# Performance work log

Hardware: AMD Instinct MI355X
Metric: run time of the kernel (lower is better)

Reference implementation:

```python
import jax, jax.numpy as jnp
import numpy as np

B, L, D, H = 8, 1024, 512, 8  # L must equal len_ for the skew trick
DH = D // H


def setup_inputs() -> dict:
    key = jax.random.key(0)
    ks = jax.random.split(key, 6)
    s = 0.02
    return {
        "x": jax.random.normal(ks[0], (B, L, D), dtype=jnp.float32),
        "Wq": jax.random.normal(ks[1], (D, D), dtype=jnp.float32) * s,
        "Wk": jax.random.normal(ks[2], (D, D), dtype=jnp.float32) * s,
        "Wv": jax.random.normal(ks[3], (D, D), dtype=jnp.float32) * s,
        "We": jax.random.normal(ks[4], (L, DH), dtype=jnp.float32) * s,  # e_projection weight: (len_, d_head)
        "Wo": jax.random.normal(ks[5], (D, D), dtype=jnp.float32) * s,
        "bo": jnp.zeros((D,), dtype=jnp.float32),
        "unused": 0,
    }


def reference(x, Wq, Wk, Wv, We, Wo, bo, unused):
    Bx, Lx, Dx = x.shape
    q = (x @ Wq.T).reshape(Bx, Lx, H, DH)  # blhd
    k = (x @ Wk.T).reshape(Bx, Lx, H, DH)
    v = (x @ Wv.T).reshape(Bx, Lx, H, DH)

    # relative-position logits: e_projection(q) then permute -> (B, H, L, len_)
    qe = jnp.einsum('blhd,ed->bhle', q, We)

    # 'skew' trick: reflect-pad right by L-1, zero-pad (right 1, bottom L-1),
    # reshape (B,H,2L-1,2L) -> (B,H,2L,2L-1), slice [:L, L-1:] -> (B,H,L,L)
    qe = jnp.pad(qe, ((0, 0), (0, 0), (0, 0), (0, Lx - 1)), mode='reflect')
    qe = jnp.pad(qe, ((0, 0), (0, 0), (0, Lx - 1), (0, 1)))
    qe = qe.reshape(Bx, H, 2 * Lx, 2 * Lx - 1)
    s_rel = qe[:, :, :Lx, Lx - 1:]

    scale = 1.0 / jnp.sqrt(jnp.asarray(DH, dtype=x.dtype))
    scores = jnp.einsum('blhd,bshd->bhls', q, k)
    A = jax.nn.softmax(scale * (scores + s_rel), axis=-1)
    V = jnp.einsum('bhls,bshd->blhd', A, v).reshape(Bx, Lx, Dx)
    return V @ Wo.T + bo
```

## Files before the change

kernel.cpp:

```cpp
#include <hip/hip_runtime.h>

#define Lc 1024
#define Dc 512
#define Hc 8
#define DHc 64

typedef __attribute__((ext_vector_type(8))) short bf16x8;
typedef __attribute__((ext_vector_type(4))) float f32x4;
typedef __attribute__((ext_vector_type(16))) float f32x16;

typedef __attribute__((address_space(1))) const unsigned int guint;
typedef __attribute__((address_space(3))) unsigned int luint;

__device__ __forceinline__ void gload_lds16(const void* g, void* l) {
    __builtin_amdgcn_global_load_lds((guint*)g, (luint*)l, 16, 0, 0);
}

__device__ __forceinline__ unsigned short f2bf(float f) {
    unsigned u = __float_as_uint(f);
    u += 0x7fffu + ((u >> 16) & 1u);
    return (unsigned short)(u >> 16);
}
__device__ __forceinline__ unsigned pk2(float a, float b) {
    return (unsigned)f2bf(a) | ((unsigned)f2bf(b) << 16);
}
__device__ __forceinline__ unsigned pk2t(float a, float b) {
    return __builtin_amdgcn_perm(__float_as_uint(b), __float_as_uint(a), 0x07060302u);
}
__device__ __forceinline__ float bf2f(unsigned short s) { return __uint_as_float(((unsigned)s) << 16); }

__device__ __forceinline__ void pl32swap(unsigned &a, unsigned &b) {
    asm volatile("v_permlane32_swap_b32 %0, %1" : "+v"(a), "+v"(b));
}
__device__ __forceinline__ unsigned alignbit(unsigned hi, unsigned lo, unsigned sh) {
    unsigned d;
    asm("v_alignbit_b32 %0, %1, %2, %3" : "=v"(d) : "v"(hi), "v"(lo), "v"(sh));
    return d;
}

__global__ void cvt_all_kernel(
    const float* __restrict__ x,  const float* __restrict__ Wq,
    const float* __restrict__ Wk, const float* __restrict__ Wv,
    const float* __restrict__ Wo, const float* __restrict__ We,
    unsigned short* __restrict__ xb,  unsigned short* __restrict__ wqb,
    unsigned short* __restrict__ wkb, unsigned short* __restrict__ wvb,
    unsigned short* __restrict__ wob, unsigned short* __restrict__ wet)
{
    int bid = blockIdx.x;
    const float* src; unsigned short* dst; size_t base;
    if      (bid < 2048) { src = x;  dst = xb;  base = (size_t)bid * 2048; }
    else if (bid < 2176) { src = Wq; dst = wqb; base = (size_t)(bid-2048) * 2048; }
    else if (bid < 2304) { src = Wk; dst = wkb; base = (size_t)(bid-2176) * 2048; }
    else if (bid < 2432) { src = Wv; dst = wvb; base = (size_t)(bid-2304) * 2048; }
    else if (bid < 2560) { src = Wo; dst = wob; base = (size_t)(bid-2432) * 2048; }
    else                 { src = We; dst = wet; base = (size_t)(bid-2560) * 2048; }
    size_t i = base + (size_t)threadIdx.x * 8;
    float4 a = *(const float4*)&src[i];
    float4 b = *(const float4*)&src[i + 4];
    uint4 o = make_uint4(pk2(a.x, a.y), pk2(a.z, a.w), pk2(b.x, b.y), pk2(b.z, b.w));
    *(uint4*)&dst[i] = o;
}

__global__ __launch_bounds__(256, 3) void proj_mfma_kernel(
    const unsigned short* __restrict__ xb,
    const unsigned short* __restrict__ wq, const unsigned short* __restrict__ wk,
    const unsigned short* __restrict__ wv,
    unsigned short* __restrict__ qo, unsigned short* __restrict__ ko,
    unsigned short* __restrict__ vtg, float qscale)
{
    const unsigned short* W;
    if (blockIdx.z == 0)      W = wq;
    else if (blockIdx.z == 1) W = wk;
    else                      W = wv;

    __shared__ unsigned short smem[128 * 136];
    unsigned short* As = smem;
    unsigned short* Bs = smem + 8192;

    const int t = threadIdx.x;
    const int lane = t & 63, w = t >> 6;
    const int lq = lane >> 4, ln = lane & 15;
    const int m0 = blockIdx.y * 128, n0 = blockIdx.x * 128;
    const int wm = (w & 1) * 64, wn = (w >> 1) * 64;
    const int srow = t >> 3;
    const int lsg  = ((t & 7) ^ ((t >> 3) & 7)) * 8;
    const int key  = ln & 7;

    f32x4 acc[4][4];
    #pragma unroll
    for (int i = 0; i < 4; i++)
        #pragma unroll
        for (int j = 0; j < 4; j++) acc[i][j] = (f32x4){0.f,0.f,0.f,0.f};

    for (int c0 = 0; c0 < 512; c0 += 64) {
        __syncthreads();
        #pragma unroll
        for (int g = 0; g < 4; g++) {
            gload_lds16(&xb[(size_t)(m0 + 32*g + srow) * 512 + c0 + lsg], &As[(32*g + srow)*64 + (t&7)*8]);
            gload_lds16(&W [(size_t)(n0 + 32*g + srow) * 512 + c0 + lsg], &Bs[(32*g + srow)*64 + (t&7)*8]);
        }
        __syncthreads();

        #pragma unroll
        for (int kk = 0; kk < 2; kk++) {
            bf16x8 af[4], bf[4];
            #pragma unroll
            for (int i = 0; i < 4; i++)
                af[i] = *(bf16x8*)&As[(wm + 16*i + ln)*64 + ((kk*4 + lq) ^ key)*8];
            #pragma unroll
            for (int j = 0; j < 4; j++)
                bf[j] = *(bf16x8*)&Bs[(wn + 16*j + ln)*64 + ((kk*4 + lq) ^ key)*8];
            #pragma unroll
            for (int i = 0; i < 4; i++)
                #pragma unroll
                for (int j = 0; j < 4; j++)
                    acc[i][j] = __builtin_amdgcn_mfma_f32_16x16x32_bf16(af[i], bf[j], acc[i][j], 0, 0, 0);
        }
    }

    if (blockIdx.z < 2) {
        unsigned short* out = (blockIdx.z == 0) ? qo : ko;
        const float osc = (blockIdx.z == 0) ? qscale : 1.0f;
        #pragma unroll
        for (int i = 0; i < 4; i++) {
            #pragma unroll
            for (int r = 0; r < 4; r++) {
                int m = m0 + wm + 16*i + 4*lq + r;
                int b = m >> 10, l = m & 1023;
                #pragma unroll
                for (int j = 0; j < 4; j++) {
                    int n = n0 + wn + 16*j + ln;
                    int h = n >> 6, dh = n & 63;
                    out[((size_t)((b*Hc + h)*Lc + l))*DHc + dh] = f2bf(acc[i][j][r] * osc);
                }
            }
        }
    } else {
        __syncthreads();
        unsigned short* Ts = smem;
        #pragma unroll
        for (int i = 0; i < 4; i++) {
            int mlb = wm + 16*i + 4*lq;
            #pragma unroll
            for (int j = 0; j < 4; j++) {
                int nl = wn + 16*j + ln;
                *(uint2*)&Ts[nl*136 + mlb] = make_uint2(pk2(acc[i][j][0], acc[i][j][1]),
                                                        pk2(acc[i][j][2], acc[i][j][3]));
            }
        }
        __syncthreads();
        const int b = m0 >> 10, l0m = m0 & 1023;
        const int nl = t >> 1, seg = (t & 1) * 64;
        const int ng = n0 + nl, h = ng >> 6, dh = ng & 63;
        unsigned short* dst = vtg + (((size_t)(b*Hc + h))*DHc + dh)*Lc + l0m + seg;
        #pragma unroll
        for (int u = 0; u < 8; u++)
            *(uint4*)&dst[8*u] = *(uint4*)&Ts[nl*136 + seg + 8*u];
    }
}

__global__ __launch_bounds__(256, 2) void out_mfma_kernel(
    const unsigned short* __restrict__ A, const unsigned short* __restrict__ W,
    const float* __restrict__ bias, float* __restrict__ out)
{
    __shared__ unsigned short As[128 * 64];
    __shared__ unsigned short Bs[64 * 64];

    const int t = threadIdx.x;
    const int lane = t & 63, w = t >> 6;
    const int lq = lane >> 4, ln = lane & 15;
    const int m0 = blockIdx.y * 128, n0 = blockIdx.x * 64;
    const int wm = (w & 1) * 64, wn = (w >> 1) * 32;
    const int srow = t >> 3;
    const int lsg  = ((t & 7) ^ ((t >> 3) & 7)) * 8;
    const int key  = ln & 7;

    f32x4 acc[4][2];
    #pragma unroll
    for (int i = 0; i < 4; i++)
        #pragma unroll
        for (int j = 0; j < 2; j++) acc[i][j] = (f32x4){0.f,0.f,0.f,0.f};

    for (int c0 = 0; c0 < 512; c0 += 64) {
        __syncthreads();
        #pragma unroll
        for (int g = 0; g < 4; g++)
            gload_lds16(&A[(size_t)(m0 + 32*g + srow) * 512 + c0 + lsg], &As[(32*g + srow)*64 + (t&7)*8]);
        #pragma unroll
        for (int g = 0; g < 2; g++)
            gload_lds16(&W[(size_t)(n0 + 32*g + srow) * 512 + c0 + lsg], &Bs[(32*g + srow)*64 + (t&7)*8]);
        __syncthreads();

        #pragma unroll
        for (int kk = 0; kk < 2; kk++) {
            bf16x8 af[4], bf[2];
            #pragma unroll
            for (int i = 0; i < 4; i++)
                af[i] = *(bf16x8*)&As[(wm + 16*i + ln)*64 + ((kk*4 + lq) ^ key)*8];
            #pragma unroll
            for (int j = 0; j < 2; j++)
                bf[j] = *(bf16x8*)&Bs[(wn + 16*j + ln)*64 + ((kk*4 + lq) ^ key)*8];
            #pragma unroll
            for (int i = 0; i < 4; i++)
                #pragma unroll
                for (int j = 0; j < 2; j++)
                    acc[i][j] = __builtin_amdgcn_mfma_f32_16x16x32_bf16(af[i], bf[j], acc[i][j], 0, 0, 0);
        }
    }

    float bb[2];
    #pragma unroll
    for (int j = 0; j < 2; j++) bb[j] = bias[n0 + wn + 16*j + ln];

    #pragma unroll
    for (int i = 0; i < 4; i++) {
        #pragma unroll
        for (int r = 0; r < 4; r++) {
            int m = m0 + wm + 16*i + 4*lq + r;
            #pragma unroll
            for (int j = 0; j < 2; j++) {
                int n = n0 + wn + 16*j + ln;
                out[(size_t)m * Dc + n] = acc[i][j][r] + bb[j];
            }
        }
    }
}

__global__ __launch_bounds__(256, 4) void attn_v13_kernel(
    const unsigned short* __restrict__ q, const unsigned short* __restrict__ k,
    const unsigned short* __restrict__ vtg, const unsigned short* __restrict__ wet,
    unsigned short* __restrict__ attn)
{
    __shared__ unsigned short smem[20480];
    unsigned short* ksp  = smem;
    unsigned short* vtp  = smem + 4096;
    unsigned short* wesp = smem + 8192;
    unsigned short* qes  = smem + 12288;

    const int t    = threadIdx.x;
    const int lane = t & 63, w = t >> 6;
    const int ln31 = lane & 31, hi = lane >> 5;
    const int si   = w >> 1;
    const int li   = w & 1;

    const int n   = blockIdx.x;
    const int xcd = n & 7, idx = n >> 3;
    const int bh  = xcd * 8 + (idx >> 4);
    const int l0  = (idx & 15) * 64;

    const unsigned short* qb  = q   + (size_t)bh * (Lc * DHc);
    const unsigned short* kb  = k   + (size_t)bh * (Lc * DHc);
    const unsigned short* vtb = vtg + (size_t)bh * (DHc * Lc);

    const int srow2 = t >> 3;
    const int lsg2  = ((t & 7) ^ ((t >> 3) & 7)) * 8;
    const int k7    = ln31 & 7;
    const int lloc  = 32*li + ln31;
    const int wkey  = (lloc & 15) << 2;
    unsigned short* qrow = &qes[lloc * 128];

    bf16x8 qf[4];
    #pragma unroll
    for (int kk = 0; kk < 4; kk++)
        qf[kk] = *(const bf16x8*)&qb[(size_t)(l0 + lloc)*64 + kk*16 + hi*8];

    const int pb0 = 15 - (l0 >> 6);

    gload_lds16(&wet[(size_t)(64*pb0 + srow2)*64 + lsg2],        &vtp [t*8]);
    gload_lds16(&wet[(size_t)(64*pb0 + 32 + srow2)*64 + lsg2],   &vtp [2048 + t*8]);
    gload_lds16(&wet[(size_t)(64*(pb0+1) + srow2)*64 + lsg2],    &wesp[t*8]);
    gload_lds16(&wet[(size_t)(64*(pb0+1) + 32 + srow2)*64 + lsg2], &wesp[2048 + t*8]);
    gload_lds16(&kb [(size_t)srow2*64 + lsg2],                   &ksp [t*8]);
    gload_lds16(&kb [(size_t)(32 + srow2)*64 + lsg2],            &ksp [2048 + t*8]);
    __syncthreads();

    {
        f32x16 qec = (f32x16){0.f,0.f,0.f,0.f,0.f,0.f,0.f,0.f,0.f,0.f,0.f,0.f,0.f,0.f,0.f,0.f};
        #pragma unroll
        for (int kk = 0; kk < 4; kk++) {
            bf16x8 wf = *(bf16x8*)&vtp[(32*si + ln31)*64 + ((2*kk + hi) ^ k7)*8];
            qec = __builtin_amdgcn_mfma_f32_32x32x16_bf16(wf, qf[kk], qec, 0, 0, 0);
        }
        const int cb = (pb0 & 1) * 64;
        #pragma unroll
        for (int g = 0; g < 4; g++) {
            const int col = (cb + 32*si + 8*g + 4*hi) ^ wkey;
            *(uint2*)&qrow[col] = make_uint2(pk2(qec[4*g], qec[4*g+1]),
                                             pk2(qec[4*g+2], qec[4*g+3]));
        }
    }

    f32x16 Ov[2];
    #pragma unroll
    for (int dt = 0; dt < 2; dt++)
        Ov[dt] = (f32x16){0.f,0.f,0.f,0.f,0.f,0.f,0.f,0.f,0.f,0.f,0.f,0.f,0.f,0.f,0.f,0.f};
    float Lacc = 0.f;

    int pbOld = pb0 - 1;

    #pragma unroll 1
    for (int s0 = 0; s0 < Lc; s0 += 64) {
        const int c0  = l0 - s0;
        const int ac0 = c0 < 0 ? -c0 : c0;
        const int pb  = (960 - ac0) >> 6;
        const int newp = (pb > pbOld) ? pb + 1 : pb;
        pbOld = pb;
        const int cb = (newp & 1) * 64;
        const bool more = (s0 < Lc - 64);
        const int nc  = c0 - 64;
        const int nac = nc < 0 ? -nc : nc;
        const int npb = (960 - nac) >> 6;
        const int nnp = (npb > pb) ? npb + 1 : npb;

        __syncthreads();

        gload_lds16(&vtb[(size_t)srow2*1024 + s0 + lsg2],        &vtp[t*8]);
        gload_lds16(&vtb[(size_t)(32 + srow2)*1024 + s0 + lsg2], &vtp[2048 + t*8]);

        {
            f32x16 qec = (f32x16){0.f,0.f,0.f,0.f,0.f,0.f,0.f,0.f,0.f,0.f,0.f,0.f,0.f,0.f,0.f,0.f};
            #pragma unroll
            for (int kk = 0; kk < 4; kk++) {
                bf16x8 wf = *(bf16x8*)&wesp[(32*si + ln31)*64 + ((2*kk + hi) ^ k7)*8];
                qec = __builtin_amdgcn_mfma_f32_32x32x16_bf16(wf, qf[kk], qec, 0, 0, 0);
            }
            #pragma unroll
            for (int g = 0; g < 4; g++) {
                const int col = (cb + 32*si + 8*g + 4*hi) ^ wkey;
                *(uint2*)&qrow[col] = make_uint2(pk2(qec[4*g], qec[4*g+1]),
                                                 pk2(qec[4*g+2], qec[4*g+3]));
            }
        }

        __syncthreads();

        if (more) {
            gload_lds16(&wet[(size_t)(64*nnp + srow2)*64 + lsg2],      &wesp[t*8]);
            gload_lds16(&wet[(size_t)(64*nnp + 32 + srow2)*64 + lsg2], &wesp[2048 + t*8]);
        }

        f32x16 sc = (f32x16){0.f,0.f,0.f,0.f,0.f,0.f,0.f,0.f,0.f,0.f,0.f,0.f,0.f,0.f,0.f,0.f};
        #pragma unroll
        for (int kk = 0; kk < 4; kk++) {
            bf16x8 kf = *(bf16x8*)&ksp[(32*si + ln31)*64 + ((2*kk + hi) ^ k7)*8];
            sc = __builtin_amdgcn_mfma_f32_32x32x16_bf16(kf, qf[kk], sc, 0, 0, 0);
        }

        float p[16];
        if (c0 >= 128 || c0 <= -64) {
            const bool asc = (c0 >= 128);
            #pragma unroll
            for (int g = 0; g < 4; g++) {
                const int dbase0 = c0 + lloc - (32*si + 8*g + 4*hi);
                const int base = asc ? (1023 - dbase0) : (1020 + dbase0);
                const int a  = (base & ~3) & 127;
                const int a2 = (a + 4) & 127;
                const uint2 w01 = *(const uint2*)&qrow[a  ^ wkey];
                const uint2 w23 = *(const uint2*)&qrow[a2 ^ wkey];
                const int off = base & 3;
                const bool oh = (off >= 2);
                const unsigned wl = oh ? w01.y : w01.x;
                const unsigned wm = oh ? w23.x : w01.y;
                const unsigned wh = oh ? w23.y : w23.x;
                const unsigned sh = (unsigned)(off & 1) * 16u;
                const unsigned r0 = alignbit(wm, wl, sh);
                const unsigned r1 = alignbit(wh, wm, sh);
                float b0, b1, b2, b3;
                if (asc) {
                    b0 = __uint_as_float(r0 << 16);
                    b1 = __uint_as_float(r0 & 0xffff0000u);
                    b2 = __uint_as_float(r1 << 16);
                    b3 = __uint_as_float(r1 & 0xffff0000u);
                } else {
                    b0 = __uint_as_float(r1 & 0xffff0000u);
                    b1 = __uint_as_float(r1 << 16);
                    b2 = __uint_as_float(r0 & 0xffff0000u);
                    b3 = __uint_as_float(r0 << 16);
                }
                p[4*g+0] = __builtin_amdgcn_exp2f(sc[4*g+0] + b0);
                p[4*g+1] = __builtin_amdgcn_exp2f(sc[4*g+1] + b1);
                p[4*g+2] = __builtin_amdgcn_exp2f(sc[4*g+2] + b2);
                p[4*g+3] = __builtin_amdgcn_exp2f(sc[4*g+3] + b3);
            }
        } else {
            #pragma unroll
            for (int g = 0; g < 4; g++) {
                const int sb = 32*si + 8*g + 4*hi;
                #pragma unroll
                for (int r = 0; r < 4; r++) {
                    int d  = c0 + lloc - sb - r;
                    int ad = d < 0 ? -d : d;
                    int m  = 1023 - ad;
                    float bias = bf2f(qrow[(m & 127) ^ wkey]);
                    p[4*g + r] = __builtin_amdgcn_exp2f(sc[4*g + r] + bias);
                }
            }
        }

        {
            float t0 = (p[0]+p[1]) + (p[2]+p[3]);
            float t1 = (p[4]+p[5]) + (p[6]+p[7]);
            float t2 = (p[8]+p[9]) + (p[10]+p[11]);
            float t3 = (p[12]+p[13]) + (p[14]+p[15]);
            Lacc += (t0 + t1) + (t2 + t3);
        }
        unsigned d0[4], d1[4];
        #pragma unroll
        for (int g = 0; g < 4; g++) {
            d0[g] = pk2t(p[4*g],     p[4*g + 1]);
            d1[g] = pk2t(p[4*g + 2], p[4*g + 3]);
        }
        bf16x8 pfr[2];
        #pragma unroll
        for (int kk = 0; kk < 2; kk++) {
            pl32swap(d0[2*kk], d0[2*kk + 1]);
            pl32swap(d1[2*kk], d1[2*kk + 1]);
            uint4 fu = make_uint4(d0[2*kk], d1[2*kk], d0[2*kk + 1], d1[2*kk + 1]);
            pfr[kk] = *(bf16x8*)&fu;
        }

        __syncthreads();

        if (more) {
            gload_lds16(&kb[(size_t)(s0 + 64 + srow2)*64 + lsg2],      &ksp[t*8]);
            gload_lds16(&kb[(size_t)(s0 + 64 + 32 + srow2)*64 + lsg2], &ksp[2048 + t*8]);
        }

        #pragma unroll
        for (int kk = 0; kk < 2; kk++)
            #pragma unroll
            for (int dt = 0; dt < 2; dt++) {
                bf16x8 vf = *(bf16x8*)&vtp[(32*dt + ln31)*64 + (((4*si + 2*kk + hi) ^ k7))*8];
                Ov[dt] = __builtin_amdgcn_mfma_f32_32x32x16_bf16(vf, pfr[kk], Ov[dt], 0, 0, 0);
            }
    }

    unsigned la = __float_as_uint(Lacc), lb = la;
    pl32swap(la, lb);
    float Lh = Lacc + __uint_as_float(hi ? la : lb);

    __syncthreads();
    float* scr = (float*)smem;
    if (si == 1) {
        #pragma unroll
        for (int dt = 0; dt < 2; dt++)
            #pragma unroll
            for (int rg = 0; rg < 16; rg++)
                scr[(dt*16 + rg)*128 + li*64 + lane] = Ov[dt][rg];
        scr[32*128 + li*64 + lane] = Lh;
    }
    __syncthreads();
    if (si == 0) {
        const float Lt = Lh + scr[32*128 + li*64 + lane];
        const float inv = 1.f / Lt;
        const int b = bh >> 3, h = bh & 7;
        const int lg = l0 + lloc;
        unsigned short* dst = attn + ((size_t)(b*Lc + lg))*Dc + h*DHc;
        #pragma unroll
        for (int dt = 0; dt < 2; dt++)
            #pragma unroll
            for (int g = 0; g < 4; g++) {
                float v0 = (Ov[dt][4*g]   + scr[(dt*16 + 4*g)*128 + li*64 + lane]) * inv;
                float v1 = (Ov[dt][4*g+1] + scr[(dt*16 + 4*g+1)*128 + li*64 + lane]) * inv;
                float v2 = (Ov[dt][4*g+2] + scr[(dt*16 + 4*g+2)*128 + li*64 + lane]) * inv;
                float v3 = (Ov[dt][4*g+3] + scr[(dt*16 + 4*g+3)*128 + li*64 + lane]) * inv;
                *(uint2*)&dst[32*dt + 8*g + 4*hi] = make_uint2(pk2(v0, v1), pk2(v2, v3));
            }
    }
}

extern "C" void kernel_launch(void* const* d_in, const int* in_sizes, int n_in,
                              void* d_out, int out_size, void* d_ws, size_t ws_size,
                              hipStream_t stream)
{
    (void)in_sizes; (void)n_in; (void)out_size; (void)ws_size;
    const float* x  = (const float*)d_in[0];
    const float* Wq = (const float*)d_in[1];
    const float* Wk = (const float*)d_in[2];
    const float* Wv = (const float*)d_in[3];
    const float* We = (const float*)d_in[4];
    const float* Wo = (const float*)d_in[5];
    const float* bo = (const float*)d_in[6];

    const size_t NT = (size_t)8 * Hc * Lc * DHc;
    unsigned short* qw  = (unsigned short*)d_ws;
    unsigned short* kw  = qw  + NT;
    unsigned short* vtg = kw  + NT;
    unsigned short* xbf = vtg + NT;
    unsigned short* awb = xbf + NT;
    unsigned short* wqb = awb + NT;
    unsigned short* wkb = wqb + 262144;
    unsigned short* wvb = wkb + 262144;
    unsigned short* wob = wvb + 262144;
    unsigned short* wet = wob + 262144;

    cvt_all_kernel<<<2592, 256, 0, stream>>>(x, Wq, Wk, Wv, Wo, We,
                                             xbf, wqb, wkb, wvb, wob, wet);
    proj_mfma_kernel<<<dim3(4, 64, 3), 256, 0, stream>>>(xbf, wqb, wkb, wvb,
                                                         qw, kw, vtg,
                                                         0.125f * 1.44269504089f);
    attn_v13_kernel<<<1024, 256, 0, stream>>>(qw, kw, vtg, wet, awb);
    out_mfma_kernel<<<dim3(8, 64), 256, 0, stream>>>(awb, wob, bo, (float*)d_out);
}
```

Measured before the change: 162.6 us.

## Fuse Q/K/V projections into one kernel sharing the x tile

Merges the three separate Q, K and V projection GEMM launches (grid z=3) into a single kernel in which each block loads one 128x64 x tile and multiplies it against 64-column tiles of Wq, Wk and Wv. Each x tile is read from global memory and staged in LDS once instead of three times. In exchange the grid shrinks from 768 to 512 blocks, the N tile per weight drops from 128 to 64, occupancy falls from 3 to 2 blocks per CU, and each thread holds more accumulators.

```diff
diff --git a/kernel.cpp b/kernel.cpp
--- a/kernel.cpp
+++ b/kernel.cpp
@@ -61,66 +61,78 @@
     *(uint4*)&dst[i] = o;
 }
 
-__global__ __launch_bounds__(256, 3) void proj_mfma_kernel(
+__global__ __launch_bounds__(256, 2) void proj_fused_kernel(
     const unsigned short* __restrict__ xb,
     const unsigned short* __restrict__ wq, const unsigned short* __restrict__ wk,
     const unsigned short* __restrict__ wv,
     unsigned short* __restrict__ qo, unsigned short* __restrict__ ko,
     unsigned short* __restrict__ vtg, float qscale)
 {
-    const unsigned short* W;
-    if (blockIdx.z == 0)      W = wq;
-    else if (blockIdx.z == 1) W = wk;
-    else                      W = wv;
-
-    __shared__ unsigned short smem[128 * 136];
+    __shared__ unsigned short smem[20480];
     unsigned short* As = smem;
-    unsigned short* Bs = smem + 8192;
+    unsigned short* Bs0 = smem + 8192;
+    unsigned short* Bs1 = smem + 12288;
+    unsigned short* Bs2 = smem + 16384;
 
     const int t = threadIdx.x;
     const int lane = t & 63, w = t >> 6;
     const int lq = lane >> 4, ln = lane & 15;
-    const int m0 = blockIdx.y * 128, n0 = blockIdx.x * 128;
-    const int wm = (w & 1) * 64, wn = (w >> 1) * 64;
+    const int m0 = blockIdx.y * 128, n0 = blockIdx.x * 64;
+    const int wm = (w & 1) * 64, wn = (w >> 1) * 32;
     const int srow = t >> 3;
     const int lsg  = ((t & 7) ^ ((t >> 3) & 7)) * 8;
     const int key  = ln & 7;
 
-    f32x4 acc[4][4];
-    #pragma unroll
-    for (int i = 0; i < 4; i++)
-        #pragma unroll
-        for (int j = 0; j < 4; j++) acc[i][j] = (f32x4){0.f,0.f,0.f,0.f};
+    f32x4 acc[3][4][2];
+    #pragma unroll
+    for (int z = 0; z < 3; z++)
+        #pragma unroll
+        for (int i = 0; i < 4; i++)
+            #pragma unroll
+            for (int j = 0; j < 2; j++) acc[z][i][j] = (f32x4){0.f,0.f,0.f,0.f};
 
     for (int c0 = 0; c0 < 512; c0 += 64) {
         __syncthreads();
         #pragma unroll
-        for (int g = 0; g < 4; g++) {
+        for (int g = 0; g < 4; g++)
             gload_lds16(&xb[(size_t)(m0 + 32*g + srow) * 512 + c0 + lsg], &As[(32*g + srow)*64 + (t&7)*8]);
-            gload_lds16(&W [(size_t)(n0 + 32*g + srow) * 512 + c0 + lsg], &Bs[(32*g + srow)*64 + (t&7)*8]);
+        #pragma unroll
+        for (int g = 0; g < 2; g++) {
+            gload_lds16(&wq[(size_t)(n0 + 32*g + srow) * 512 + c0 + lsg], &Bs0[(32*g + srow)*64 + (t&7)*8]);
+            gload_lds16(&wk[(size_t)(n0 + 32*g + srow) * 512 + c0 + lsg], &Bs1[(32*g + srow)*64 + (t&7)*8]);
+            gload_lds16(&wv[(size_t)(n0 + 32*g + srow) * 512 + c0 + lsg], &Bs2[(32*g + srow)*64 + (t&7)*8]);
         }
         __syncthreads();
 
         #pragma unroll
         for (int kk = 0; kk < 2; kk++) {
-            bf16x8 af[4], bf[4];
+            bf16x8 af[4];
             #pragma unroll
             for (int i = 0; i < 4; i++)
                 af[i] = *(bf16x8*)&As[(wm + 16*i + ln)*64 + ((kk*4 + lq) ^ key)*8];
-            #pragma unroll
-            for (int j = 0; j < 4; j++)
-                bf[j] = *(bf16x8*)&Bs[(wn + 16*j + ln)*64 + ((kk*4 + lq) ^ key)*8];
-            #pragma unroll
-            for (int i = 0; i < 4; i++)
+
+            unsigned short* Bz[3] = {Bs0, Bs1, Bs2};
+            #pragma unroll
+            for (int z = 0; z < 3; z++) {
+                bf16x8 bf[2];
                 #pragma unroll
-                for (int j = 0; j < 4; j++)
-                    acc[i][j] = __builtin_amdgcn_mfma_f32_16x16x32_bf16(af[i], bf[j], acc[i][j], 0, 0, 0);
-        }
-    }
-
-    if (blockIdx.z < 2) {
-        unsigned short* out = (blockIdx.z == 0) ? qo : ko;
-        const float osc = (blockIdx.z == 0) ? qscale : 1.0f;
+                for (int j = 0; j < 2; j++)
+                    bf[j] = *(bf16x8*)&Bz[z][(wn + 16*j + ln)*64 + ((kk*4 + lq) ^ key)*8];
+                #pragma unroll
+                for (int i = 0; i < 4; i++)
+                    #pragma unroll
+                    for (int j = 0; j < 2; j++)
+                        acc[z][i][j] = __builtin_amdgcn_mfma_f32_16x16x32_bf16(af[i], bf[j], acc[z][i][j], 0, 0, 0);
+            }
+        }
+    }
+
+    const int h = n0 >> 6;
+
+    #pragma unroll
+    for (int z = 0; z < 2; z++) {
+        unsigned short* out = z ? ko : qo;
+        const float osc = z ? 1.0f : qscale;
         #pragma unroll
         for (int i = 0; i < 4; i++) {
             #pragma unroll
@@ -128,33 +140,33 @@
                 int m = m0 + wm + 16*i + 4*lq + r;
                 int b = m >> 10, l = m & 1023;
                 #pragma unroll
-                for (int j = 0; j < 4; j++) {
-                    int n = n0 + wn + 16*j + ln;
-                    int h = n >> 6, dh = n & 63;
-                    out[((size_t)((b*Hc + h)*Lc + l))*DHc + dh] = f2bf(acc[i][j][r] * osc);
+                for (int j = 0; j < 2; j++) {
+                    int dh = wn + 16*j + ln;
+                    out[((size_t)((b*Hc + h)*Lc + l))*DHc + dh] = f2bf(acc[z][i][j][r] * osc);
                 }
             }
         }
-    } else {
-        __syncthreads();
-        unsigned short* Ts = smem;
-        #pragma unroll
-        for (int i = 0; i < 4; i++) {
-            int mlb = wm + 16*i + 4*lq;
-            #pragma unroll
-            for (int j = 0; j < 4; j++) {
-                int nl = wn + 16*j + ln;
-                *(uint2*)&Ts[nl*136 + mlb] = make_uint2(pk2(acc[i][j][0], acc[i][j][1]),
-                                                        pk2(acc[i][j][2], acc[i][j][3]));
-            }
-        }
-        __syncthreads();
+    }
+
+    __syncthreads();
+    unsigned short* Ts = smem;
+    #pragma unroll
+    for (int i = 0; i < 4; i++) {
+        int mlb = wm + 16*i + 4*lq;
+        #pragma unroll
+        for (int j = 0; j < 2; j++) {
+            int nl = wn + 16*j + ln;
+            *(uint2*)&Ts[nl*136 + mlb] = make_uint2(pk2(acc[2][i][j][0], acc[2][i][j][1]),
+                                                    pk2(acc[2][i][j][2], acc[2][i][j][3]));
+        }
+    }
+    __syncthreads();
+    {
         const int b = m0 >> 10, l0m = m0 & 1023;
-        const int nl = t >> 1, seg = (t & 1) * 64;
-        const int ng = n0 + nl, h = ng >> 6, dh = ng & 63;
-        unsigned short* dst = vtg + (((size_t)(b*Hc + h))*DHc + dh)*Lc + l0m + seg;
-        #pragma unroll
-        for (int u = 0; u < 8; u++)
+        const int nl = t >> 2, seg = (t & 3) * 32;
+        unsigned short* dst = vtg + (((size_t)(b*Hc + h))*DHc + nl)*Lc + l0m + seg;
+        #pragma unroll
+        for (int u = 0; u < 4; u++)
             *(uint4*)&dst[8*u] = *(uint4*)&Ts[nl*136 + seg + 8*u];
     }
 }
@@ -496,9 +508,9 @@
 
     cvt_all_kernel<<<2592, 256, 0, stream>>>(x, Wq, Wk, Wv, Wo, We,
                                              xbf, wqb, wkb, wvb, wob, wet);
-    proj_mfma_kernel<<<dim3(4, 64, 3), 256, 0, stream>>>(xbf, wqb, wkb, wvb,
-                                                         qw, kw, vtg,
-                                                         0.125f * 1.44269504089f);
+    proj_fused_kernel<<<dim3(8, 64), 256, 0, stream>>>(xbf, wqb, wkb, wvb,
+                                                       qw, kw, vtg,
+                                                       0.125f * 1.44269504089f);
     attn_v13_kernel<<<1024, 256, 0, stream>>>(qw, kw, vtg, wet, awb);
     out_mfma_kernel<<<dim3(8, 64), 256, 0, stream>>>(awb, wob, bo, (float*)d_out);
 }
```

Result: no change. 161.7 us (-0.6%).
